# Kernel optimization log

Hardware: AMD Instinct MI355X
Metric: run time of the kernel (lower is better)

The kernel has to match this reference:

```python
import jax, jax.numpy as jnp
import numpy as np

N = 100000        # nodes
E = 3200000       # edges (avg degree 32)
D = 16            # feature dim
LAM = 1.0
ALP = 1.0 / (LAM + 1.0)   # alp=0 default -> 1/(lam+1)
PROP_STEP = 5


def setup_inputs() -> dict:
    key = jax.random.key(0)
    k1, k2, k3 = jax.random.split(key, 3)
    edge_index = jax.random.randint(k1, (2, E), 0, N, dtype=jnp.int32)
    X = jax.random.normal(k2, (N, D), dtype=jnp.float32)
    train_mask = jax.random.randint(k3, (N,), 0, 2, dtype=jnp.int32) > 0
    return {"edge_index": edge_index, "X": X, "train_mask": train_mask}


def reference(edge_index, X, train_mask):
    src, dst = edge_index[0], edge_index[1]
    # g.edata['w'] = ones; g.ndata['deg'] = in_degrees
    deg = jax.ops.segment_sum(jnp.ones((E,), X.dtype), dst, num_segments=N)
    dinv = jnp.where(deg > 0, jax.lax.rsqrt(jnp.maximum(deg, 1.0)), 0.0)  # D^{-1/2}, 0-deg -> 0

    def norm_AX(Y):
        # D^{-1/2} A D^{-1/2} Y  via gather over src, scatter-add into dst
        h = (Y * dinv[:, None])[src]                       # [E, D]
        agg = jax.ops.segment_sum(h, dst, num_segments=N)  # [N, D]
        return agg * dinv[:, None]

    mask = train_mask[:, None]
    Y = X
    for _ in range(PROP_STEP):
        # PropagateNoPrecond: (1 - alp - alp*lam) Y + alp*lam * Ahat Y + alp * X
        Y = (1.0 - ALP - ALP * LAM) * Y + (ALP * LAM) * norm_AX(Y) + ALP * X
        # error=True branch: post_step clamp then reset train nodes to X
        Y = jnp.clip(Y, -1.0, 1.0)
        Y = jnp.where(mask, X, Y)
    return Y
```

## Files before the change

kernel.cpp:

```cpp
#include <hip/hip_runtime.h>

#define NN 100000
#define NE 3200000
#define DD 16
#define NB 782
#define NBP 1024
#define CHUNK 8192
#define NCHUNK ((NE + CHUNK - 1) / CHUNK)
#define PREPB ((NN + NBP - 1) / NBP)
#define BCAP2 4864
#define BMW 3128

constexpr float LAM   = 1.0f;
constexpr float ALP   = 1.0f / (LAM + 1.0f);
constexpr float GAMMA = ALP * LAM;
constexpr float S0    = 127.0f / 6.0f;
constexpr float INVS0 = 6.0f / 127.0f;
constexpr float INVS1 = 1.0f / 127.0f;

__global__ __launch_bounds__(NBP) void bucket_scatter(
        const int* __restrict__ srcs, const int* __restrict__ dsts,
        int* __restrict__ bcnt, unsigned int* __restrict__ pk,
        const int* __restrict__ mask, unsigned long long* __restrict__ bm64,
        int* __restrict__ uidx, int* __restrict__ ucount) {
    __shared__ int lh[NBP];
    __shared__ int off[NBP];
    __shared__ int gb[NBP];
    __shared__ int wred[16];
    __shared__ unsigned long long spair[CHUNK];
    int t = threadIdx.x;

    if (blockIdx.x >= NCHUNK) {
        int n0 = (int)(blockIdx.x - NCHUNK) * NBP + t;
        int lane = t & 63;
        bool m = (n0 < NN) && (mask[n0] != 0);
        unsigned long long balm = __ballot(m);
        int w = n0 >> 6;
        if (lane == 0 && w < 1564) bm64[w] = balm;
        bool u = (n0 < NN) && !m;
        unsigned long long bal = __ballot(u);
        int cnt = __popcll(bal);
        if (lane == 0) wred[t >> 6] = cnt;
        __syncthreads();
        if (t == 0) {
            int s = 0;
            #pragma unroll
            for (int w2 = 0; w2 < 16; ++w2) { int c = wred[w2]; wred[w2] = s; s += c; }
            gb[0] = (s > 0) ? atomicAdd(ucount, s) : 0;
        }
        __syncthreads();
        if (u) {
            int pos = gb[0] + wred[t >> 6] +
                      __popcll(bal & ((1ull << lane) - 1ull));
            uidx[n0] = pos;
        }
        return;
    }

    int base = blockIdx.x * CHUNK;
    int n = NE - base; if (n > CHUNK) n = CHUNK;

    lh[t] = 0;
    __syncthreads();

    int e0 = 8 * t;
    int dreg[8];
    int rk[8];
    bool full = (e0 + 8 <= n);
    if (full) {
        int4 a = *(const int4*)&dsts[base + e0];
        int4 bq = *(const int4*)&dsts[base + e0 + 4];
        dreg[0] = a.x;  dreg[1] = a.y;  dreg[2] = a.z;  dreg[3] = a.w;
        dreg[4] = bq.x; dreg[5] = bq.y; dreg[6] = bq.z; dreg[7] = bq.w;
        #pragma unroll
        for (int k = 0; k < 8; ++k) rk[k] = atomicAdd(&lh[dreg[k] >> 7], 1);
    } else {
        #pragma unroll
        for (int k = 0; k < 8; ++k) {
            int i = e0 + k;
            dreg[k] = (i < n) ? dsts[base + i] : -1;
        }
        #pragma unroll
        for (int k = 0; k < 8; ++k)
            rk[k] = (dreg[k] >= 0) ? atomicAdd(&lh[dreg[k] >> 7], 1) : 0;
    }
    __syncthreads();

    int v = lh[t];
    int x = v;
    #pragma unroll
    for (int s = 1; s < 64; s <<= 1) {
        int y = __shfl_up(x, s, 64);
        if ((t & 63) >= s) x += y;
    }
    if ((t & 63) == 63) wred[t >> 6] = x;
    __syncthreads();
    if (t < 16) {
        int ww = wred[t];
        int xx = ww;
        #pragma unroll
        for (int s = 1; s < 16; s <<= 1) {
            int y = __shfl_up(xx, s, 16);
            if (t >= s) xx += y;
        }
        wred[t] = xx - ww;
    }
    __syncthreads();
    x += wred[t >> 6];
    int cnt  = v;
    int excl = x - v;
    off[t] = excl;
    if (cnt > 0) gb[t] = t * BCAP2 + atomicAdd(&bcnt[t << 4], cnt) - excl;
    __syncthreads();

    if (full) {
        int4 a = *(const int4*)&srcs[base + e0];
        int4 bq = *(const int4*)&srcs[base + e0 + 4];
        int sreg[8];
        sreg[0] = a.x;  sreg[1] = a.y;  sreg[2] = a.z;  sreg[3] = a.w;
        sreg[4] = bq.x; sreg[5] = bq.y; sreg[6] = bq.z; sreg[7] = bq.w;
        #pragma unroll
        for (int k = 0; k < 8; ++k) {
            unsigned int d = (unsigned int)dreg[k];
            int p = off[d >> 7] + rk[k];
            spair[p] = ((unsigned long long)d << 32) | (unsigned int)sreg[k];
        }
    } else {
        #pragma unroll
        for (int k = 0; k < 8; ++k) {
            int i = e0 + k;
            if (i < n) {
                unsigned int d = (unsigned int)dreg[k];
                unsigned int s = (unsigned int)srcs[base + i];
                int p = off[d >> 7] + rk[k];
                spair[p] = ((unsigned long long)d << 32) | s;
            }
        }
    }
    __syncthreads();

    unsigned long long wv[8];
    #pragma unroll
    for (int k = 0; k < 8; ++k) {
        int p = t + k * NBP;
        wv[k] = (p < n) ? spair[p] : 0ull;
    }
    #pragma unroll
    for (int k = 0; k < 8; ++k) {
        int p = t + k * NBP;
        if (p < n) {
            unsigned int d = (unsigned int)(wv[k] >> 32);
            int bb = (int)(d >> 7);
            pk[gb[bb] + p] = ((d & 127u) << 17) | (unsigned int)wv[k];
        }
    }
}

static __device__ inline unsigned int qb8(float xv, float sc) {
    float q = fminf(fmaxf(xv * sc, -127.0f), 127.0f);
    return (unsigned int)(__float2int_rn(q) + 128) & 255u;
}

__global__ void fine_csr(unsigned int* __restrict__ pk,
                         const int* __restrict__ bcnt,
                         const float* __restrict__ X,
                         const unsigned int* __restrict__ bitmap,
                         const int* __restrict__ uidx,
                         int* __restrict__ row_start,
                         uint4* __restrict__ ndesc,
                         unsigned char* __restrict__ Za,
                         unsigned char* __restrict__ Zb,
                         float* __restrict__ Y) {
    __shared__ int lh[256], off[256];
    __shared__ int wred[4];
    __shared__ float sdi[128];
    __shared__ unsigned int bmp[BMW];
    __shared__ int sbuf[BCAP2];
    int b  = blockIdx.x;
    int t  = threadIdx.x;
    int b0 = b * BCAP2;
    int cnt = bcnt[b << 4];
    lh[t] = 0;
    for (int i0 = 4 * t; i0 < BMW; i0 += 1024) {
        uint4 q = *(const uint4*)&bitmap[i0];
        *(uint4*)&bmp[i0] = q;
    }
    __syncthreads();

    unsigned int sv[20];
    unsigned int kr[20];
    #pragma unroll
    for (int it = 0; it < 5; ++it) {
        int i0 = 4 * t + it * 1024;
        if (i0 + 4 <= cnt) {
            uint4 q = *(const uint4*)&pk[b0 + i0];
            unsigned int vv[4] = {q.x, q.y, q.z, q.w};
            #pragma unroll
            for (int k = 0; k < 4; ++k) {
                unsigned int s = vv[k] & 0x1FFFFu;
                int mb = (bmp[s >> 5] >> (s & 31)) & 1;
                unsigned int key = ((vv[k] >> 17) << 1) | (mb ? 0u : 1u);
                unsigned int r = (unsigned int)atomicAdd(&lh[key], 1);
                sv[it * 4 + k] = s;
                kr[it * 4 + k] = (key << 16) | r;
            }
        } else {
            #pragma unroll
            for (int k = 0; k < 4; ++k) {
                int i = i0 + k;
                if (i < cnt) {
                    unsigned int v = pk[b0 + i];
                    unsigned int s = v & 0x1FFFFu;
                    int mb = (bmp[s >> 5] >> (s & 31)) & 1;
                    unsigned int key = ((v >> 17) << 1) | (mb ? 0u : 1u);
                    unsigned int r = (unsigned int)atomicAdd(&lh[key], 1);
                    sv[it * 4 + k] = s;
                    kr[it * 4 + k] = (key << 16) | r;
                } else {
                    sv[it * 4 + k] = 0u;
                    kr[it * 4 + k] = 0u;
                }
            }
        }
    }
    __syncthreads();
    int v = lh[t];
    int x = v;
    #pragma unroll
    for (int s = 1; s < 64; s <<= 1) {
        int y = __shfl_up(x, s, 64);
        if ((t & 63) >= s) x += y;
    }
    if ((t & 63) == 63) wred[t >> 6] = x;
    __syncthreads();
    if (t < 4) {
        int ww = wred[t];
        int xx = ww;
        #pragma unroll
        for (int s = 1; s < 4; s <<= 1) {
            int y = __shfl_up(xx, s, 4);
            if (t >= s) xx += y;
        }
        wred[t] = xx - ww;
    }
    __syncthreads();
    x += wred[t >> 6];
    off[t] = x;
    int myexcl = x - v;
    __syncthreads();
    if (t < 128) {
        int cs = lh[2 * t], cd = lh[2 * t + 1];
        int es = off[2 * t] - cs;
        int ed = off[2 * t + 1] - cd;
        int c  = cs + cd;
        int dst = (b << 7) + t;
        float di = (c > 0) ? rsqrtf((float)c) : 0.0f;
        sdi[t] = di;
        if (dst < NN) {
            row_start[dst] = b0 + es;
            if (!((bmp[dst >> 5] >> (dst & 31)) & 1)) {
                int ix = uidx[dst];
                ndesc[ix] = make_uint4((unsigned int)dst,
                                       (unsigned int)(b0 + ed),
                                       (unsigned int)(b0 + ed + cd),
                                       __float_as_uint(di));
            }
        }
    }
    __syncthreads();
    off[t] = myexcl;
    __syncthreads();

    #pragma unroll
    for (int it = 0; it < 5; ++it) {
        #pragma unroll
        for (int k = 0; k < 4; ++k) {
            int i = 4 * t + it * 1024 + k;
            if (i < cnt) {
                unsigned int w = kr[it * 4 + k];
                int p = off[w >> 16] + (int)(w & 0xFFFFu);
                sbuf[p] = (int)sv[it * 4 + k];
            }
        }
    }
    __syncthreads();

    for (int i0 = 4 * t; i0 < cnt; i0 += 1024) {
        if (i0 + 4 <= cnt) {
            int4 q = *(const int4*)&sbuf[i0];
            *(int4*)&pk[b0 + i0] = q;
        } else {
            for (int k = 0; k < 4; ++k) {
                int i = i0 + k;
                if (i < cnt) pk[b0 + i] = (unsigned int)sbuf[i];
            }
        }
    }

    {
        int ldst = t >> 1;
        int ff0  = (t & 1) * 8;
        int dst  = (b << 7) + ldst;
        if (dst < NN) {
            float4 xa = *(const float4*)&X[dst * DD + ff0];
            float4 xb = *(const float4*)&X[dst * DD + ff0 + 4];
            float sc = sdi[ldst] * S0;
            unsigned int w0 = qb8(xa.x, sc) | (qb8(xa.y, sc) << 8) |
                              (qb8(xa.z, sc) << 16) | (qb8(xa.w, sc) << 24);
            unsigned int w1 = qb8(xb.x, sc) | (qb8(xb.y, sc) << 8) |
                              (qb8(xb.z, sc) << 16) | (qb8(xb.w, sc) << 24);
            *(uint2*)(Za + dst * DD + ff0) = make_uint2(w0, w1);
            if ((bmp[dst >> 5] >> (dst & 31)) & 1) {
                *(float4*)&Y[dst * DD + ff0]     = xa;
                *(float4*)&Y[dst * DD + ff0 + 4] = xb;
            }
        }
    }
    if (b == 0 && t < DD) {
        Za[NN * DD + t] = 128;
        Zb[NN * DD + t] = 128;
    }
}

static __device__ inline void fold16(float* acc, int ln) {
    {
        int sel = ln & 1;
        #pragma unroll
        for (int k = 0; k < 8; ++k) {
            float mine   = sel ? acc[k + 8] : acc[k];
            float theirs = sel ? acc[k]     : acc[k + 8];
            acc[k] = mine + __shfl_xor(theirs, 1, 16);
        }
    }
    {
        int sel = (ln >> 1) & 1;
        #pragma unroll
        for (int k = 0; k < 4; ++k) {
            float mine   = sel ? acc[k + 4] : acc[k];
            float theirs = sel ? acc[k]     : acc[k + 4];
            acc[k] = mine + __shfl_xor(theirs, 2, 16);
        }
    }
    {
        int sel = (ln >> 2) & 1;
        #pragma unroll
        for (int k = 0; k < 2; ++k) {
            float mine   = sel ? acc[k + 2] : acc[k];
            float theirs = sel ? acc[k]     : acc[k + 2];
            acc[k] = mine + __shfl_xor(theirs, 4, 16);
        }
    }
    {
        int sel = (ln >> 3) & 1;
        float mine   = sel ? acc[1] : acc[0];
        float theirs = sel ? acc[0] : acc[1];
        acc[0] = mine + __shfl_xor(theirs, 8, 16);
    }
}

static __device__ inline void accum16(const unsigned int* __restrict__ csr,
                                      const uint4* __restrict__ Zt,
                                      int lo, int hi, int ln, float* acc) {
    int p = lo + ln;
    int s = (p < hi) ? (int)csr[p] : NN;
    for (int i = lo; i < hi; i += 16) {
        uint4 r = Zt[s];
        int pn = i + 16 + ln;
        int sn = (pn < hi) ? (int)csr[pn] : NN;
        acc[0]  += (float)(r.x & 255u);         acc[1]  += (float)((r.x >> 8) & 255u);
        acc[2]  += (float)((r.x >> 16) & 255u); acc[3]  += (float)(r.x >> 24);
        acc[4]  += (float)(r.y & 255u);         acc[5]  += (float)((r.y >> 8) & 255u);
        acc[6]  += (float)((r.y >> 16) & 255u); acc[7]  += (float)(r.y >> 24);
        acc[8]  += (float)(r.z & 255u);         acc[9]  += (float)((r.z >> 8) & 255u);
        acc[10] += (float)((r.z >> 16) & 255u); acc[11] += (float)(r.z >> 24);
        acc[12] += (float)(r.w & 255u);         acc[13] += (float)((r.w >> 8) & 255u);
        acc[14] += (float)((r.w >> 16) & 255u); acc[15] += (float)(r.w >> 24);
        s = sn;
    }
}

__global__ void gather_kernel(const unsigned int* __restrict__ csr,
                              const int* __restrict__ row_start,
                              const uint4* __restrict__ ndesc,
                              const float* __restrict__ X,
                              float* __restrict__ Sst,
                              const int* __restrict__ ucount,
                              const unsigned char* __restrict__ Zrow,
                              unsigned char* __restrict__ Zout,
                              float* __restrict__ Yo,
                              float invS, int first, int last) {
    int tid = blockIdx.x * blockDim.x + threadIdx.x;
    int idx = tid >> 4;
    int ln  = tid & 15;
    if (idx >= *ucount) return;
    uint4 nd = ndesc[idx];
    int node = (int)nd.x;
    int mid  = (int)nd.y;
    int hi   = (int)nd.z;
    float di = __uint_as_float(nd.w);
    int fp = 8 * (ln & 1) + 4 * ((ln >> 1) & 1) + 2 * ((ln >> 2) & 1) + ((ln >> 3) & 1);
    const uint4* Zt = (const uint4*)Zrow;

    float s0;
    float g = GAMMA * di * invS;
    if (first) {
        int lo = row_start[node];
        float accS[16];
        #pragma unroll
        for (int k = 0; k < 16; ++k) accS[k] = 0.0f;
        accum16(csr, Zt, lo, mid, ln, accS);
        fold16(accS, ln);
        int nchS = (mid - lo + 15) >> 4;
        float bias = 2048.0f * (float)nchS;
        float x0 = __builtin_nontemporal_load(&X[node * DD + fp]);
        s0 = g * (accS[0] - bias) + ALP * x0;
        Sst[node * DD + fp] = s0;
    } else {
        s0 = Sst[node * DD + fp];
    }

    float acc[16];
    #pragma unroll
    for (int k = 0; k < 16; ++k) acc[k] = 0.0f;
    accum16(csr, Zt, mid, hi, ln, acc);
    fold16(acc, ln);
    int nchD = (hi - mid + 15) >> 4;
    float v0 = s0 + g * (acc[0] - 2048.0f * (float)nchD);
    v0 = fminf(fmaxf(v0, -1.0f), 1.0f);
    if (last) {
        Yo[node * DD + fp] = v0;
    } else {
        int q0 = __float2int_rn(v0 * di * 127.0f) + 128;
        Zout[node * DD + fp] = (unsigned char)q0;
    }
}

extern "C" void kernel_launch(void* const* d_in, const int* in_sizes, int n_in,
                              void* d_out, int out_size, void* d_ws, size_t ws_size,
                              hipStream_t stream) {
    const int*   edge_index = (const int*)d_in[0];
    const float* X          = (const float*)d_in[1];
    const int*   mask       = (const int*)d_in[2];

    const int* srcs = edge_index;
    const int* dsts = edge_index + NE;

    float* Y = (float*)d_out;

    unsigned char* Za = (unsigned char*)d_ws;
    unsigned char* Zb = Za + (NN + 1) * DD;
    float* Sst        = (float*)(Zb + (NN + 1) * DD);
    unsigned int* pk  = (unsigned int*)(Sst + NN * DD);
    int*   bcnt      = (int*)(pk + NB * BCAP2);
    int*   ucount    = bcnt + NBP * 16;
    int*   pad       = ucount + 1;
    unsigned int* bitmap = (unsigned int*)(pad + 3);
    int*   uidx      = (int*)(bitmap + BMW);
    int*   row_start = uidx + NN;
    uint4* ndesc     = (uint4*)(row_start + NN);

    (void)hipMemsetAsync(bcnt, 0, (NBP * 16 + 4) * sizeof(int), stream);

    bucket_scatter<<<NCHUNK + PREPB, NBP, 0, stream>>>(
        srcs, dsts, bcnt, pk, mask, (unsigned long long*)bitmap, uidx, ucount);
    fine_csr<<<NB, 256, 0, stream>>>(pk, bcnt, X, bitmap, uidx, row_start,
                                     ndesc, Za, Zb, Y);

    const unsigned char* zin  = Za;
    unsigned char*       zout = Zb;
    for (int t = 0; t < 5; ++t) {
        int first = (t == 0);
        int last  = (t == 4);
        gather_kernel<<<(NN * 16) / 256, 256, 0, stream>>>(
            pk, row_start, ndesc, X, Sst, ucount,
            zin, zout, Y, first ? INVS0 : INVS1, first, last);
        const unsigned char* tmp = zout;
        zout = (unsigned char*)zin;
        zin  = tmp;
    }
}
```

Baseline: 101.2 us.

## Use 32 lanes per node with grid-stride loop in gather kernel

The gather kernel now assigns 32 lanes to each node instead of 16. Each lane fetches one neighbor's 16-byte quantized row, and an extra shuffle step folds the two half-groups. The launch switches from one thread group per node to a fixed grid with a grid-stride loop over the active node list. This is meant to raise memory-level parallelism per node and cut block launch overhead and tail imbalance. The cost is that half the lanes sit idle during the final write, and short rows leave more lanes padding.

```diff
diff --git a/kernel.cpp b/kernel.cpp
--- a/kernel.cpp
+++ b/kernel.cpp
@@ -10,6 +10,7 @@
 #define PREPB ((NN + NBP - 1) / NBP)
 #define BCAP2 4864
 #define BMW 3128
+#define GGRID 7168
 
 constexpr float LAM   = 1.0f;
 constexpr float ALP   = 1.0f / (LAM + 1.0f);
@@ -322,7 +323,7 @@
     }
 }
 
-static __device__ inline void fold16(float* acc, int ln) {
+static __device__ inline void fold32(float* acc, int ln) {
     {
         int sel = ln & 1;
         #pragma unroll
@@ -356,16 +357,17 @@
         float theirs = sel ? acc[0] : acc[1];
         acc[0] = mine + __shfl_xor(theirs, 8, 16);
     }
-}
-
-static __device__ inline void accum16(const unsigned int* __restrict__ csr,
+    acc[0] += __shfl_xor(acc[0], 16, 32);
+}
+
+static __device__ inline void accum32(const unsigned int* __restrict__ csr,
                                       const uint4* __restrict__ Zt,
                                       int lo, int hi, int ln, float* acc) {
     int p = lo + ln;
     int s = (p < hi) ? (int)csr[p] : NN;
-    for (int i = lo; i < hi; i += 16) {
+    for (int i = lo; i < hi; i += 32) {
         uint4 r = Zt[s];
-        int pn = i + 16 + ln;
+        int pn = i + 32 + ln;
         int sn = (pn < hi) ? (int)csr[pn] : NN;
         acc[0]  += (float)(r.x & 255u);         acc[1]  += (float)((r.x >> 8) & 255u);
         acc[2]  += (float)((r.x >> 16) & 255u); acc[3]  += (float)(r.x >> 24);
@@ -379,7 +381,8 @@
     }
 }
 
-__global__ void gather_kernel(const unsigned int* __restrict__ csr,
+__global__ __launch_bounds__(256) void gather_kernel(
+                              const unsigned int* __restrict__ csr,
                               const int* __restrict__ row_start,
                               const uint4* __restrict__ ndesc,
                               const float* __restrict__ X,
@@ -389,49 +392,56 @@
                               unsigned char* __restrict__ Zout,
                               float* __restrict__ Yo,
                               float invS, int first, int last) {
-    int tid = blockIdx.x * blockDim.x + threadIdx.x;
-    int idx = tid >> 4;
-    int ln  = tid & 15;
-    if (idx >= *ucount) return;
-    uint4 nd = ndesc[idx];
-    int node = (int)nd.x;
-    int mid  = (int)nd.y;
-    int hi   = (int)nd.z;
-    float di = __uint_as_float(nd.w);
-    int fp = 8 * (ln & 1) + 4 * ((ln >> 1) & 1) + 2 * ((ln >> 2) & 1) + ((ln >> 3) & 1);
+    int uc = *ucount;
+    int tg = threadIdx.x >> 5;
+    int ln = threadIdx.x & 31;
+    int l4 = ln & 15;
+    int fp = 8 * (l4 & 1) + 4 * ((l4 >> 1) & 1) + 2 * ((l4 >> 2) & 1) + ((l4 >> 3) & 1);
     const uint4* Zt = (const uint4*)Zrow;
 
-    float s0;
-    float g = GAMMA * di * invS;
-    if (first) {
-        int lo = row_start[node];
-        float accS[16];
-        #pragma unroll
-        for (int k = 0; k < 16; ++k) accS[k] = 0.0f;
-        accum16(csr, Zt, lo, mid, ln, accS);
-        fold16(accS, ln);
-        int nchS = (mid - lo + 15) >> 4;
-        float bias = 2048.0f * (float)nchS;
-        float x0 = __builtin_nontemporal_load(&X[node * DD + fp]);
-        s0 = g * (accS[0] - bias) + ALP * x0;
-        Sst[node * DD + fp] = s0;
-    } else {
-        s0 = Sst[node * DD + fp];
-    }
-
-    float acc[16];
-    #pragma unroll
-    for (int k = 0; k < 16; ++k) acc[k] = 0.0f;
-    accum16(csr, Zt, mid, hi, ln, acc);
-    fold16(acc, ln);
-    int nchD = (hi - mid + 15) >> 4;
-    float v0 = s0 + g * (acc[0] - 2048.0f * (float)nchD);
-    v0 = fminf(fmaxf(v0, -1.0f), 1.0f);
-    if (last) {
-        Yo[node * DD + fp] = v0;
-    } else {
-        int q0 = __float2int_rn(v0 * di * 127.0f) + 128;
-        Zout[node * DD + fp] = (unsigned char)q0;
+    for (int idx = blockIdx.x * 8 + tg; idx < uc; idx += gridDim.x * 8) {
+        uint4 nd = ndesc[idx];
+        int node = (int)nd.x;
+        int mid  = (int)nd.y;
+        int hi   = (int)nd.z;
+        float di = __uint_as_float(nd.w);
+        float g = GAMMA * di * invS;
+
+        float s0 = 0.0f;
+        if (first) {
+            int lo = row_start[node];
+            float accS[16];
+            #pragma unroll
+            for (int k = 0; k < 16; ++k) accS[k] = 0.0f;
+            accum32(csr, Zt, lo, mid, ln, accS);
+            fold32(accS, ln);
+            int nchS = (mid - lo + 31) >> 5;
+            float bias = 4096.0f * (float)nchS;
+            if (ln < 16) {
+                float x0 = __builtin_nontemporal_load(&X[node * DD + fp]);
+                s0 = g * (accS[0] - bias) + ALP * x0;
+                Sst[node * DD + fp] = s0;
+            }
+        } else {
+            if (ln < 16) s0 = Sst[node * DD + fp];
+        }
+
+        float acc[16];
+        #pragma unroll
+        for (int k = 0; k < 16; ++k) acc[k] = 0.0f;
+        accum32(csr, Zt, mid, hi, ln, acc);
+        fold32(acc, ln);
+        int nchD = (hi - mid + 31) >> 5;
+        if (ln < 16) {
+            float v0 = s0 + g * (acc[0] - 4096.0f * (float)nchD);
+            v0 = fminf(fmaxf(v0, -1.0f), 1.0f);
+            if (last) {
+                Yo[node * DD + fp] = v0;
+            } else {
+                int q0 = __float2int_rn(v0 * di * 127.0f) + 128;
+                Zout[node * DD + fp] = (unsigned char)q0;
+            }
+        }
     }
 }
 
@@ -471,7 +481,7 @@
     for (int t = 0; t < 5; ++t) {
         int first = (t == 0);
         int last  = (t == 4);
-        gather_kernel<<<(NN * 16) / 256, 256, 0, stream>>>(
+        gather_kernel<<<GGRID, 256, 0, stream>>>(
             pk, row_start, ndesc, X, Sst, ucount,
             zin, zout, Y, first ? INVS0 : INVS1, first, last);
         const unsigned char* tmp = zout;
```

Result: slower. 109.1 us (+7.9%).
